# Kernel optimization log

Measured on AMD Instinct MI355X. Metric: run time of the kernel, lower is better.

Reference implementation:

```python
import jax, jax.numpy as jnp
import numpy as np

V = 32000   # vocab_size
HD = 512    # num_hiddens
B = 32      # batch
T = 128     # seq_len


def setup_inputs() -> dict:
    key = jax.random.key(0)
    ks = jax.random.split(key, 11)
    s_in = 1.0 / np.sqrt(V + HD)   # torch Linear default init bound
    s_out = 1.0 / np.sqrt(HD)

    def lin_w(k, out_f, in_f, s):
        return jax.random.uniform(k, (out_f, in_f), jnp.float32, -s, s)

    def lin_b(k, out_f, s):
        return jax.random.uniform(k, (out_f,), jnp.float32, -s, s)

    return {
        "X": jax.random.randint(ks[0], (B, T), 0, V),
        "H": jnp.zeros((B, HD), jnp.float32),
        "C": jnp.zeros((B, HD), jnp.float32),
        "Wf": lin_w(ks[1], HD, V + HD, s_in), "bf": lin_b(ks[2], HD, s_in),
        "Wi": lin_w(ks[3], HD, V + HD, s_in), "bi": lin_b(ks[4], HD, s_in),
        "Wo": lin_w(ks[5], HD, V + HD, s_in), "bo": lin_b(ks[6], HD, s_in),
        "Wc": lin_w(ks[7], HD, V + HD, s_in), "bc": lin_b(ks[8], HD, s_in),
        "Wy": lin_w(ks[9], V, HD, s_out),     "by": lin_b(ks[10], V, s_out),
    }


def reference(X, H, C, Wf, bf, Wi, bi, Wo, bo, Wc, bc, Wy, by):
    # X: [B, T] int tokens. Transposed to time-major like torch's X.T.
    Xt = X.T  # [T, B]
    hd = H.shape[1]
    v = Wf.shape[1] - hd

    def split(W):
        return W[:, :v], W[:, v:]  # input part, hidden part

    Wfx, Wfh = split(Wf)
    Wix, Wih = split(Wi)
    Wox, Woh = split(Wo)
    Wcx, Wch = split(Wc)

    # one_hot(x) @ Wx^T == row-gather of Wx^T: same math, no wasted compute.
    Ef = jnp.take(Wfx.T, Xt, axis=0) + bf  # [T, B, HD]
    Ei = jnp.take(Wix.T, Xt, axis=0) + bi
    Eo = jnp.take(Wox.T, Xt, axis=0) + bo
    Ec = jnp.take(Wcx.T, Xt, axis=0) + bc

    def step(carry, e):
        h, c = carry
        ef, ei, eo, ec = e
        f = jax.nn.sigmoid(ef + h @ Wfh.T)
        i = jax.nn.sigmoid(ei + h @ Wih.T)
        o = jax.nn.sigmoid(eo + h @ Woh.T)
        c_tilde = jnp.tanh(ec + h @ Wch.T)
        c = f * c + i * c_tilde
        h = o * jnp.tanh(c)
        return (h, c), h

    (H, C), Hs = jax.lax.scan(step, (H, C), (Ef, Ei, Eo, Ec))  # Hs: [T, B, HD]

    # per-step Y = h2out(H), then torch.cat(outputs, dim=0) -> [T*B, V]
    Y = Hs.reshape(-1, hd) @ Wy.T + by
    return Y, (H, C)
```

## Files before the change

### kernel.cpp

```cpp
#include <hip/hip_runtime.h>
#include <hip/hip_bf16.h>

#define V  32000
#define HD 512
#define BB 32
#define TT 128
#define VH 32512
#define LBLK 8
#define NBLK 256
#define GBLK (NBLK - LBLK)
#define NTILE (32 * 125)

typedef short  short8  __attribute__((ext_vector_type(8)));
typedef unsigned short u16x8 __attribute__((ext_vector_type(8)));
typedef unsigned short u16x4 __attribute__((ext_vector_type(4)));
typedef float  f32x4   __attribute__((ext_vector_type(4)));

__device__ __forceinline__ unsigned short bf16_rne(float f) {
  unsigned u = __builtin_bit_cast(unsigned, f);
  u += 0x7FFFu + ((u >> 16) & 1u);
  return (unsigned short)(u >> 16);
}

__device__ __forceinline__ void gload_lds16(const void* g, void* l) {
  __builtin_amdgcn_global_load_lds((const __attribute__((address_space(1))) void*)g,
                                   (__attribute__((address_space(3))) void*)l, 16, 0, 0);
}

__device__ __forceinline__ float sigf(float x) {
  return 1.0f / (1.0f + __expf(-x));
}
__device__ __forceinline__ float tanhf_fast(float x) {
  return 1.0f - 2.0f / (1.0f + __expf(2.0f * x));
}

__device__ __forceinline__ unsigned aload(const unsigned* p) {
  return __hip_atomic_load(p, __ATOMIC_RELAXED, __HIP_MEMORY_SCOPE_AGENT);
}
__device__ __forceinline__ void astore(unsigned* p, unsigned v) {
  __hip_atomic_store(p, v, __ATOMIC_RELAXED, __HIP_MEMORY_SCOPE_AGENT);
}
__device__ __forceinline__ unsigned aadd(unsigned* p, unsigned v) {
  return __hip_atomic_fetch_add(p, v, __ATOMIC_RELAXED, __HIP_MEMORY_SCOPE_AGENT);
}

__global__ void __launch_bounds__(512, 2) fused_all(
    const int* __restrict__ X,
    const float* __restrict__ Hin,
    const float* __restrict__ Cin,
    const float* __restrict__ Wf, const float* __restrict__ bfp,
    const float* __restrict__ Wi, const float* __restrict__ bip,
    const float* __restrict__ Wo, const float* __restrict__ bop,
    const float* __restrict__ Wc, const float* __restrict__ bcp,
    const float* __restrict__ Wy, const float* __restrict__ by,
    float* __restrict__ E,
    unsigned short* __restrict__ HsM1,
    unsigned short* __restrict__ Wyb,
    float* __restrict__ outHC,
    unsigned* __restrict__ bar,
    unsigned* __restrict__ bar2,
    unsigned* __restrict__ wbar,
    unsigned* __restrict__ eflag,
    unsigned* __restrict__ lticket,
    unsigned* __restrict__ gticket,
    float* __restrict__ Y)
{
  __shared__ __align__(16) char smem[75776];
  __shared__ int sh_role;

  const int tid = threadIdx.x;
  const int wid = tid >> 6, lane = tid & 63;
  const int fr = lane & 15, ko = lane >> 4;

  unsigned short* Hs = HsM1 + BB * HD;

  if (tid == 0) {
    unsigned xcd;
    asm volatile("s_getreg_b32 %0, hwreg(20, 0, 32)" : "=s"(xcd));
    int role = -1;
    if (xcd == 0) {
      const unsigned s = aadd(lticket, 1u);
      if (s < (unsigned)LBLK) role = (int)s;
    }
    if (role < 0) {
      const unsigned g = aadd(gticket, 1u);
      role = -(int)g - 2;
    }
    sh_role = role;
  }
  __syncthreads();
  const int role = sh_role;

  if (role >= 0) {
    short* hl = (short*)smem;
    float (*Pl)[BB][68] = (float(*)[BB][68])(smem + 32768);
    float (*cl)[64]     = (float(*)[64])(smem + 32768 + 34816);

    const int blk = role;
    const int g = wid & 3, qg = wid >> 2;

    const float* Wg = (g == 0) ? Wf : (g == 1) ? Wi : (g == 2) ? Wo : Wc;
    short8 wreg[2][16];
    #pragma unroll
    for (int n = 0; n < 2; ++n) {
      const int q = blk * 64 + qg * 32 + n * 16 + fr;
      const float* rowp = Wg + (size_t)q * VH + V;
      #pragma unroll
      for (int kk = 0; kk < 16; ++kk) {
        const float4 lo = *(const float4*)(rowp + kk * 32 + ko * 8);
        const float4 hi = *(const float4*)(rowp + kk * 32 + ko * 8 + 4);
        short8 w;
        w[0] = (short)bf16_rne(lo.x); w[1] = (short)bf16_rne(lo.y);
        w[2] = (short)bf16_rne(lo.z); w[3] = (short)bf16_rne(lo.w);
        w[4] = (short)bf16_rne(hi.x); w[5] = (short)bf16_rne(hi.y);
        w[6] = (short)bf16_rne(hi.z); w[7] = (short)bf16_rne(hi.w);
        wreg[n][kk] = w;
      }
    }

    const int e0 = tid * 4;
    const int eb = e0 >> 6, ql = e0 & 63;
    const int qglob = blk * 64 + ql;
    {
      const f32x4 c4 = *(const f32x4*)(Cin + eb * HD + qglob);
      *(f32x4*)&cl[eb][ql] = c4;
      const f32x4 h4 = *(const f32x4*)(Hin + eb * HD + qglob);
      u16x4 hq;
      #pragma unroll
      for (int j = 0; j < 4; ++j) hq[j] = bf16_rne(h4[j]);
      *(u16x4*)(HsM1 + (size_t)eb * HD + qglob) = hq;
    }
    __syncthreads();

    if (tid == 0) {
      aadd(bar, 1u);
      while (aload(bar) < (unsigned)LBLK) {}
      while (aload(&eflag[0]) < 1u) {}
    }
    __syncthreads();

    int abase[2], asw[2];
    #pragma unroll
    for (int m = 0; m < 2; ++m) {
      const int r = m * 16 + fr;
      abase[m] = r * 1024;
      asw[m] = (r & 7) << 4;
    }

    for (int t = 0; t < TT; ++t) {
      if (t > 0) {
        __syncthreads();
        if (tid == 0) {
          aadd(bar, 1u);
          const unsigned tgt = (unsigned)(LBLK * (t + 1));
          while (aload(bar) < tgt) {}
          while (aload(&eflag[t]) < 1u) {}
          if (blk == 0 && (t & 7) == 0) {
            __threadfence();
            astore(bar2, (unsigned)t);
          }
        }
        __syncthreads();
      }

      const char* hsrc = (const char*)(HsM1 + (size_t)t * (BB * HD));
      #pragma unroll
      for (int is = 0; is < 4; ++is) {
        const int i = is * 512 + tid;
        const int sb = (i >> 6) * 1024 + (((i & 63) * 16) ^ (((i >> 6) & 7) << 4));
        gload_lds16(hsrc + sb, (char*)hl + (size_t)(is * 512 + (tid & ~63)) * 16);
      }

      const float* Eb = E + ((size_t)t * 4) * BB * HD;
      const f32x4 ef = *(const f32x4*)(Eb + (size_t)(0 * BB + eb) * HD + qglob);
      const f32x4 ei = *(const f32x4*)(Eb + (size_t)(1 * BB + eb) * HD + qglob);
      const f32x4 eo = *(const f32x4*)(Eb + (size_t)(2 * BB + eb) * HD + qglob);
      const f32x4 ec = *(const f32x4*)(Eb + (size_t)(3 * BB + eb) * HD + qglob);

      __syncthreads();

      f32x4 acc[2][2];
      #pragma unroll
      for (int m = 0; m < 2; ++m)
        #pragma unroll
        for (int n = 0; n < 2; ++n)
          acc[m][n] = (f32x4){0.f, 0.f, 0.f, 0.f};

      #pragma unroll
      for (int kk = 0; kk < 16; ++kk) {
        const int off = kk * 64 + ko * 16;
        const short8 a0 = *(const short8*)((const char*)hl + abase[0] + (off ^ asw[0]));
        const short8 a1 = *(const short8*)((const char*)hl + abase[1] + (off ^ asw[1]));
        acc[0][0] = __builtin_amdgcn_mfma_f32_16x16x32_bf16(a0, wreg[0][kk], acc[0][0], 0, 0, 0);
        acc[1][0] = __builtin_amdgcn_mfma_f32_16x16x32_bf16(a1, wreg[0][kk], acc[1][0], 0, 0, 0);
        acc[0][1] = __builtin_amdgcn_mfma_f32_16x16x32_bf16(a0, wreg[1][kk], acc[0][1], 0, 0, 0);
        acc[1][1] = __builtin_amdgcn_mfma_f32_16x16x32_bf16(a1, wreg[1][kk], acc[1][1], 0, 0, 0);
      }

      #pragma unroll
      for (int m = 0; m < 2; ++m)
        #pragma unroll
        for (int n = 0; n < 2; ++n)
          #pragma unroll
          for (int j = 0; j < 4; ++j)
            Pl[g][m * 16 + ko * 4 + j][qg * 32 + n * 16 + fr] = acc[m][n][j];
      __syncthreads();

      const f32x4 pf4 = *(const f32x4*)&Pl[0][eb][ql];
      const f32x4 pi4 = *(const f32x4*)&Pl[1][eb][ql];
      const f32x4 po4 = *(const f32x4*)&Pl[2][eb][ql];
      const f32x4 pc4 = *(const f32x4*)&Pl[3][eb][ql];
      const f32x4 cold = *(const f32x4*)&cl[eb][ql];
      f32x4 cnew, hnew;
      u16x4 hq;
      #pragma unroll
      for (int j = 0; j < 4; ++j) {
        const float fg = sigf(pf4[j] + ef[j]);
        const float ig = sigf(pi4[j] + ei[j]);
        const float og = sigf(po4[j] + eo[j]);
        const float ct = tanhf_fast(pc4[j] + ec[j]);
        const float cn = fg * cold[j] + ig * ct;
        const float hv = og * tanhf_fast(cn);
        cnew[j] = cn;
        hnew[j] = hv;
        hq[j] = bf16_rne(hv);
      }
      *(f32x4*)&cl[eb][ql] = cnew;
      *(u16x4*)(Hs + ((size_t)t * BB + eb) * HD + qglob) = hq;
      if (t == TT - 1) {
        *(f32x4*)(outHC + (size_t)eb * HD + qglob) = hnew;
        *(f32x4*)(outHC + (size_t)BB * HD + (size_t)eb * HD + qglob) = cnew;
      }
    }

    __syncthreads();
    if (tid == 0) {
      aadd(bar, 1u);
      if (blk == 0) {
        while (aload(bar) < (unsigned)(LBLK * (TT + 1))) {}
        __threadfence();
        astore(bar2, (unsigned)TT);
      }
    }
  } else {
    unsigned short* As = (unsigned short*)smem;
    unsigned short* Bs = (unsigned short*)(smem + 16384);
    int* xs            = (int*)(smem + 49152);

    const int gid = -role - 2;

    if (gid < TT) {
      const int tch = gid;
      if (tid < BB) xs[tid] = X[tid * TT + tch];
      __syncthreads();
      const int q = tid;
      float* Erow = E + ((size_t)tch * 4) * BB * HD;
      #pragma unroll
      for (int g = 0; g < 4; ++g) {
        const float* W = (g == 0) ? Wf : (g == 1) ? Wi : (g == 2) ? Wo : Wc;
        const float* bsrc = (g == 0) ? bfp : (g == 1) ? bip : (g == 2) ? bop : bcp;
        const float bias = bsrc[q];
        const float* wq = W + (size_t)q * VH;
        #pragma unroll 4
        for (int b = 0; b < BB; ++b) {
          const float v = __builtin_nontemporal_load(wq + xs[b]);
          Erow[(size_t)(g * BB + b) * HD + q] = v + bias;
        }
      }
      __syncthreads();
      if (tid == 0) {
        __threadfence();
        astore(&eflag[tch], 1u);
      }
    }

    {
      const size_t n = (size_t)V * HD;
      for (size_t i = ((size_t)gid * 512 + tid) * 8; i < n;
           i += (size_t)GBLK * 512 * 8) {
        const f32x4 a = __builtin_nontemporal_load((const f32x4*)(Wy + i));
        const f32x4 b = __builtin_nontemporal_load((const f32x4*)(Wy + i + 4));
        u16x8 o;
        o[0] = bf16_rne(a[0]); o[1] = bf16_rne(a[1]); o[2] = bf16_rne(a[2]); o[3] = bf16_rne(a[3]);
        o[4] = bf16_rne(b[0]); o[5] = bf16_rne(b[1]); o[6] = bf16_rne(b[2]); o[7] = bf16_rne(b[3]);
        *(u16x8*)(Wyb + i) = o;
      }
      __syncthreads();
      if (tid == 0) {
        __threadfence();
        aadd(wbar, 1u);
        while (aload(wbar) < (unsigned)GBLK)
          __builtin_amdgcn_s_sleep(2);
      }
      __syncthreads();
    }

    const int wr = wid >> 2, wc = wid & 3;

    for (int tile = gid; tile < NTILE; tile += GBLK) {
      const int bm = tile / 125, bn = tile % 125;
      const int row0 = bm << 7, col0 = bn << 8;

      if (tid == 0) {
        const unsigned need = (unsigned)(4 * bm + 4);
        while (aload(bar2) < need)
          __builtin_amdgcn_s_sleep(2);
      }
      __syncthreads();

      f32x4 acc[4][4];
      #pragma unroll
      for (int m = 0; m < 4; ++m)
        #pragma unroll
        for (int n = 0; n < 4; ++n)
          acc[m][n] = (f32x4){0.f, 0.f, 0.f, 0.f};

      for (int kt = 0; kt < 8; ++kt) {
        const int k0 = kt << 6;
        #pragma unroll
        for (int is = 0; is < 2; ++is) {
          const int id = is * 512 + tid;
          const int r = id >> 3;
          const int c = (id & 7) ^ (r & 7);
          gload_lds16(Hs + (size_t)(row0 + r) * 512 + k0 + c * 8,
                      &As[(is * 512 + (tid & ~63)) * 8]);
        }
        #pragma unroll
        for (int is = 0; is < 4; ++is) {
          const int id = is * 512 + tid;
          const int r = id >> 3;
          const int c = (id & 7) ^ (r & 7);
          gload_lds16(Wyb + (size_t)(col0 + r) * 512 + k0 + c * 8,
                      &Bs[(is * 512 + (tid & ~63)) * 8]);
        }
        __syncthreads();
        #pragma unroll
        for (int kk = 0; kk < 2; ++kk) {
          short8 af[4], bfr[4];
          #pragma unroll
          for (int m = 0; m < 4; ++m) {
            const int r = (wr << 6) + (m << 4) + fr;
            const int c = ((kk << 2) | ko) ^ (r & 7);
            af[m] = *(const short8*)&As[r * 64 + c * 8];
          }
          #pragma unroll
          for (int n = 0; n < 4; ++n) {
            const int r = (wc << 6) + (n << 4) + fr;
            const int c = ((kk << 2) | ko) ^ (r & 7);
            bfr[n] = *(const short8*)&Bs[r * 64 + c * 8];
          }
          #pragma unroll
          for (int m = 0; m < 4; ++m)
            #pragma unroll
            for (int n = 0; n < 4; ++n)
              acc[m][n] = __builtin_amdgcn_mfma_f32_16x16x32_bf16(
                  af[m], bfr[n], acc[m][n], 0, 0, 0);
        }
        __syncthreads();
      }

      const int rgrp = lane >> 4;
      #pragma unroll
      for (int n = 0; n < 4; ++n) {
        const int col = col0 + (wc << 6) + (n << 4) + fr;
        const float bias = by[col];
        #pragma unroll
        for (int m = 0; m < 4; ++m) {
          const int rowb = row0 + (wr << 6) + (m << 4) + (rgrp << 2);
          #pragma unroll
          for (int j = 0; j < 4; ++j) {
            __builtin_nontemporal_store(acc[m][n][j] + bias,
                                        &Y[(size_t)(rowb + j) * V + col]);
          }
        }
      }
    }
  }
}

extern "C" void kernel_launch(void* const* d_in, const int* in_sizes, int n_in,
                              void* d_out, int out_size, void* d_ws, size_t ws_size,
                              hipStream_t stream)
{
  const int*   X  = (const int*)  d_in[0];
  const float* H  = (const float*)d_in[1];
  const float* C  = (const float*)d_in[2];
  const float* Wf = (const float*)d_in[3];
  const float* bf = (const float*)d_in[4];
  const float* Wi = (const float*)d_in[5];
  const float* bi = (const float*)d_in[6];
  const float* Wo = (const float*)d_in[7];
  const float* bo = (const float*)d_in[8];
  const float* Wc = (const float*)d_in[9];
  const float* bc = (const float*)d_in[10];
  const float* Wy = (const float*)d_in[11];
  const float* by = (const float*)d_in[12];

  float* Y = (float*)d_out;
  float* outHC = Y + (size_t)TT * BB * V;

  char* ws = (char*)d_ws;
  float* E              = (float*)ws;
  unsigned short* Wyb   = (unsigned short*)(ws + 33554432);
  unsigned short* HsM1  = (unsigned short*)(ws + 66322432);
  unsigned* bar         = (unsigned*)(ws + 70549504);
  unsigned* bar2        = (unsigned*)(ws + 70549504 + 64);
  unsigned* wbar        = (unsigned*)(ws + 70549504 + 128);
  unsigned* lticket     = (unsigned*)(ws + 70549504 + 192);
  unsigned* gticket     = (unsigned*)(ws + 70549504 + 256);
  unsigned* eflag       = (unsigned*)(ws + 70549504 + 320);

  (void)hipMemsetAsync(bar, 0, 1024, stream);

  {
    const int* X_p = X;
    const float *H_p = H, *C_p = C;
    const float *Wf_p = Wf, *bf_p = bf, *Wi_p = Wi, *bi_p = bi;
    const float *Wo_p = Wo, *bo_p = bo, *Wc_p = Wc, *bc_p = bc;
    const float *Wy_p = Wy, *by_p = by;
    float* E_p = E;
    unsigned short* HsM1_p = HsM1;
    unsigned short* Wyb_p = Wyb;
    float* outHC_p = outHC;
    unsigned *bar_p = bar, *bar2_p = bar2, *wbar_p = wbar, *eflag_p = eflag;
    unsigned *lticket_p = lticket, *gticket_p = gticket;
    float* Y_p = Y;
    void* args[] = {(void*)&X_p, (void*)&H_p, (void*)&C_p,
                    (void*)&Wf_p, (void*)&bf_p, (void*)&Wi_p, (void*)&bi_p,
                    (void*)&Wo_p, (void*)&bo_p, (void*)&Wc_p, (void*)&bc_p,
                    (void*)&Wy_p, (void*)&by_p,
                    (void*)&E_p, (void*)&HsM1_p, (void*)&Wyb_p, (void*)&outHC_p,
                    (void*)&bar_p, (void*)&bar2_p, (void*)&wbar_p, (void*)&eflag_p,
                    (void*)&lticket_p, (void*)&gticket_p,
                    (void*)&Y_p};
    (void)hipLaunchCooperativeKernel((void*)fused_all, dim3(NBLK), dim3(512), args, 0, stream);
  }
}
```

Measured before the change: 900.3 us.

## Replace LSTM step barrier with per-block flags and register-resident gate layout

```diff
diff --git a/kernel.cpp b/kernel.cpp
--- a/kernel.cpp
+++ b/kernel.cpp
@@ -57,9 +57,9 @@
     unsigned short* __restrict__ HsM1,
     unsigned short* __restrict__ Wyb,
     float* __restrict__ outHC,
-    unsigned* __restrict__ bar,
     unsigned* __restrict__ bar2,
     unsigned* __restrict__ wbar,
+    unsigned* __restrict__ bflag,
     unsigned* __restrict__ eflag,
     unsigned* __restrict__ lticket,
     unsigned* __restrict__ gticket,
@@ -71,6 +71,7 @@
   const int tid = threadIdx.x;
   const int wid = tid >> 6, lane = tid & 63;
   const int fr = lane & 15, ko = lane >> 4;
+  const int rowgrp = lane >> 4;
 
   unsigned short* Hs = HsM1 + BB * HD;
 
@@ -92,19 +93,16 @@
   const int role = sh_role;
 
   if (role >= 0) {
-    short* hl = (short*)smem;
-    float (*Pl)[BB][68] = (float(*)[BB][68])(smem + 32768);
-    float (*cl)[64]     = (float(*)[64])(smem + 32768 + 34816);
-
     const int blk = role;
-    const int g = wid & 3, qg = wid >> 2;
-
-    const float* Wg = (g == 0) ? Wf : (g == 1) ? Wi : (g == 2) ? Wo : Wc;
+    const int qb = blk * 64 + wid * 8;
+
     short8 wreg[2][16];
     #pragma unroll
-    for (int n = 0; n < 2; ++n) {
-      const int q = blk * 64 + qg * 32 + n * 16 + fr;
-      const float* rowp = Wg + (size_t)q * VH + V;
+    for (int mt = 0; mt < 2; ++mt) {
+      const int qA = qb + mt * 4 + (fr >> 2);
+      const int gA = fr & 3;
+      const float* WgA = (gA == 0) ? Wf : (gA == 1) ? Wi : (gA == 2) ? Wo : Wc;
+      const float* rowp = WgA + (size_t)qA * VH + V;
       #pragma unroll
       for (int kk = 0; kk < 16; ++kk) {
         const float4 lo = *(const float4*)(rowp + kk * 32 + ko * 8);
@@ -114,130 +112,106 @@
         w[2] = (short)bf16_rne(lo.z); w[3] = (short)bf16_rne(lo.w);
         w[4] = (short)bf16_rne(hi.x); w[5] = (short)bf16_rne(hi.y);
         w[6] = (short)bf16_rne(hi.z); w[7] = (short)bf16_rne(hi.w);
-        wreg[n][kk] = w;
-      }
-    }
-
-    const int e0 = tid * 4;
-    const int eb = e0 >> 6, ql = e0 & 63;
-    const int qglob = blk * 64 + ql;
-    {
-      const f32x4 c4 = *(const f32x4*)(Cin + eb * HD + qglob);
-      *(f32x4*)&cl[eb][ql] = c4;
-      const f32x4 h4 = *(const f32x4*)(Hin + eb * HD + qglob);
-      u16x4 hq;
-      #pragma unroll
-      for (int j = 0; j < 4; ++j) hq[j] = bf16_rne(h4[j]);
-      *(u16x4*)(HsM1 + (size_t)eb * HD + qglob) = hq;
-    }
+        wreg[mt][kk] = w;
+      }
+    }
+
+    float creg[2][2];
+    #pragma unroll
+    for (int mt = 0; mt < 2; ++mt)
+      #pragma unroll
+      for (int nt = 0; nt < 2; ++nt) {
+        const int b = nt * 16 + fr;
+        const int q = qb + mt * 4 + rowgrp;
+        creg[mt][nt] = Cin[b * HD + q];
+        HsM1[(size_t)b * HD + q] = bf16_rne(Hin[b * HD + q]);
+      }
     __syncthreads();
-
-    if (tid == 0) {
-      aadd(bar, 1u);
-      while (aload(bar) < (unsigned)LBLK) {}
-      while (aload(&eflag[0]) < 1u) {}
-    }
-    __syncthreads();
-
-    int abase[2], asw[2];
-    #pragma unroll
-    for (int m = 0; m < 2; ++m) {
-      const int r = m * 16 + fr;
-      abase[m] = r * 1024;
-      asw[m] = (r & 7) << 4;
-    }
+    if (wid == 0 && lane == 0) astore(&bflag[blk * 16], 1u);
 
     for (int t = 0; t < TT; ++t) {
-      if (t > 0) {
-        __syncthreads();
-        if (tid == 0) {
-          aadd(bar, 1u);
-          const unsigned tgt = (unsigned)(LBLK * (t + 1));
-          while (aload(bar) < tgt) {}
-          while (aload(&eflag[t]) < 1u) {}
-          if (blk == 0 && (t & 7) == 0) {
-            __threadfence();
-            astore(bar2, (unsigned)t);
+      {
+        const unsigned* pa = (lane < 8) ? (bflag + lane * 16)
+                           : (lane == 8) ? (eflag + t) : bflag;
+        const unsigned tgt = (lane < 8) ? (unsigned)(t + 1)
+                           : (lane == 8) ? 4u : 0u;
+        while (true) {
+          const unsigned v = aload(pa);
+          if (__all((int)(v >= tgt))) break;
+        }
+      }
+      if (blk == 0 && wid == 0 && lane == 0 && t && !(t & 7)) {
+        __threadfence();
+        astore(bar2, (unsigned)t);
+      }
+
+      f32x4 eld[2][2];
+      {
+        const float* Ebase = E + (size_t)t * BB * HD * 4;
+        #pragma unroll
+        for (int mt = 0; mt < 2; ++mt)
+          #pragma unroll
+          for (int nt = 0; nt < 2; ++nt) {
+            const int b = nt * 16 + fr;
+            const int q = qb + mt * 4 + rowgrp;
+            eld[mt][nt] = *(const f32x4*)(Ebase + ((size_t)b * HD + q) * 4);
           }
-        }
-        __syncthreads();
-      }
-
-      const char* hsrc = (const char*)(HsM1 + (size_t)t * (BB * HD));
-      #pragma unroll
-      for (int is = 0; is < 4; ++is) {
-        const int i = is * 512 + tid;
-        const int sb = (i >> 6) * 1024 + (((i & 63) * 16) ^ (((i >> 6) & 7) << 4));
-        gload_lds16(hsrc + sb, (char*)hl + (size_t)(is * 512 + (tid & ~63)) * 16);
-      }
-
-      const float* Eb = E + ((size_t)t * 4) * BB * HD;
-      const f32x4 ef = *(const f32x4*)(Eb + (size_t)(0 * BB + eb) * HD + qglob);
-      const f32x4 ei = *(const f32x4*)(Eb + (size_t)(1 * BB + eb) * HD + qglob);
-      const f32x4 eo = *(const f32x4*)(Eb + (size_t)(2 * BB + eb) * HD + qglob);
-      const f32x4 ec = *(const f32x4*)(Eb + (size_t)(3 * BB + eb) * HD + qglob);
-
-      __syncthreads();
-
+      }
+
+      const char* hb0 = (const char*)HsM1 + (size_t)t * (BB * HD * 2)
+                      + fr * (HD * 2) + ko * 16;
+      const char* hb1 = hb0 + 16 * (HD * 2);
       f32x4 acc[2][2];
       #pragma unroll
-      for (int m = 0; m < 2; ++m)
-        #pragma unroll
-        for (int n = 0; n < 2; ++n)
-          acc[m][n] = (f32x4){0.f, 0.f, 0.f, 0.f};
-
+      for (int mt = 0; mt < 2; ++mt)
+        #pragma unroll
+        for (int nt = 0; nt < 2; ++nt)
+          acc[mt][nt] = (f32x4){0.f, 0.f, 0.f, 0.f};
       #pragma unroll
       for (int kk = 0; kk < 16; ++kk) {
-        const int off = kk * 64 + ko * 16;
-        const short8 a0 = *(const short8*)((const char*)hl + abase[0] + (off ^ asw[0]));
-        const short8 a1 = *(const short8*)((const char*)hl + abase[1] + (off ^ asw[1]));
-        acc[0][0] = __builtin_amdgcn_mfma_f32_16x16x32_bf16(a0, wreg[0][kk], acc[0][0], 0, 0, 0);
-        acc[1][0] = __builtin_amdgcn_mfma_f32_16x16x32_bf16(a1, wreg[0][kk], acc[1][0], 0, 0, 0);
-        acc[0][1] = __builtin_amdgcn_mfma_f32_16x16x32_bf16(a0, wreg[1][kk], acc[0][1], 0, 0, 0);
-        acc[1][1] = __builtin_amdgcn_mfma_f32_16x16x32_bf16(a1, wreg[1][kk], acc[1][1], 0, 0, 0);
-      }
-
-      #pragma unroll
-      for (int m = 0; m < 2; ++m)
-        #pragma unroll
-        for (int n = 0; n < 2; ++n)
-          #pragma unroll
-          for (int j = 0; j < 4; ++j)
-            Pl[g][m * 16 + ko * 4 + j][qg * 32 + n * 16 + fr] = acc[m][n][j];
-      __syncthreads();
-
-      const f32x4 pf4 = *(const f32x4*)&Pl[0][eb][ql];
-      const f32x4 pi4 = *(const f32x4*)&Pl[1][eb][ql];
-      const f32x4 po4 = *(const f32x4*)&Pl[2][eb][ql];
-      const f32x4 pc4 = *(const f32x4*)&Pl[3][eb][ql];
-      const f32x4 cold = *(const f32x4*)&cl[eb][ql];
-      f32x4 cnew, hnew;
-      u16x4 hq;
-      #pragma unroll
-      for (int j = 0; j < 4; ++j) {
-        const float fg = sigf(pf4[j] + ef[j]);
-        const float ig = sigf(pi4[j] + ei[j]);
-        const float og = sigf(po4[j] + eo[j]);
-        const float ct = tanhf_fast(pc4[j] + ec[j]);
-        const float cn = fg * cold[j] + ig * ct;
-        const float hv = og * tanhf_fast(cn);
-        cnew[j] = cn;
-        hnew[j] = hv;
-        hq[j] = bf16_rne(hv);
-      }
-      *(f32x4*)&cl[eb][ql] = cnew;
-      *(u16x4*)(Hs + ((size_t)t * BB + eb) * HD + qglob) = hq;
-      if (t == TT - 1) {
-        *(f32x4*)(outHC + (size_t)eb * HD + qglob) = hnew;
-        *(f32x4*)(outHC + (size_t)BB * HD + (size_t)eb * HD + qglob) = cnew;
-      }
-    }
-
-    __syncthreads();
-    if (tid == 0) {
-      aadd(bar, 1u);
-      if (blk == 0) {
-        while (aload(bar) < (unsigned)(LBLK * (TT + 1))) {}
+        const short8 b0 = *(const short8*)(hb0 + kk * 64);
+        const short8 b1 = *(const short8*)(hb1 + kk * 64);
+        acc[0][0] = __builtin_amdgcn_mfma_f32_16x16x32_bf16(wreg[0][kk], b0, acc[0][0], 0, 0, 0);
+        acc[0][1] = __builtin_amdgcn_mfma_f32_16x16x32_bf16(wreg[0][kk], b1, acc[0][1], 0, 0, 0);
+        acc[1][0] = __builtin_amdgcn_mfma_f32_16x16x32_bf16(wreg[1][kk], b0, acc[1][0], 0, 0, 0);
+        acc[1][1] = __builtin_amdgcn_mfma_f32_16x16x32_bf16(wreg[1][kk], b1, acc[1][1], 0, 0, 0);
+      }
+
+      unsigned short* hstore = HsM1 + (size_t)(t + 1) * (BB * HD);
+      #pragma unroll
+      for (int mt = 0; mt < 2; ++mt)
+        #pragma unroll
+        for (int nt = 0; nt < 2; ++nt) {
+          const int b = nt * 16 + fr;
+          const int q = qb + mt * 4 + rowgrp;
+          const f32x4 a = acc[mt][nt];
+          const f32x4 e4 = eld[mt][nt];
+          const float fg = sigf(a[0] + e4[0]);
+          const float ig = sigf(a[1] + e4[1]);
+          const float og = sigf(a[2] + e4[2]);
+          const float ct = tanhf_fast(a[3] + e4[3]);
+          const float cn = fg * creg[mt][nt] + ig * ct;
+          const float hv = og * tanhf_fast(cn);
+          creg[mt][nt] = cn;
+          hstore[(size_t)b * HD + q] = bf16_rne(hv);
+          if (t == TT - 1) {
+            outHC[(size_t)b * HD + q] = hv;
+            outHC[(size_t)BB * HD + b * HD + q] = cn;
+          }
+        }
+
+      __syncthreads();
+      if (wid == 0 && lane == 0) astore(&bflag[blk * 16], (unsigned)(t + 2));
+    }
+
+    if (wid == 0) {
+      const unsigned* pa = (lane < 8) ? (bflag + lane * 16) : bflag;
+      const unsigned tgt = (lane < 8) ? (unsigned)(TT + 1) : 0u;
+      while (true) {
+        const unsigned v = aload(pa);
+        if (__all((int)(v >= tgt))) break;
+      }
+      if (blk == 0 && lane == 0) {
         __threadfence();
         astore(bar2, (unsigned)TT);
       }
@@ -249,28 +223,28 @@
 
     const int gid = -role - 2;
 
-    if (gid < TT) {
-      const int tch = gid;
-      if (tid < BB) xs[tid] = X[tid * TT + tch];
+    for (int u = gid; u < 4 * TT; u += GBLK) {
+      const int tg = u >> 2, qtr = u & 3;
+      if (tid < 8) xs[tid] = X[(qtr * 8 + tid) * TT + tg];
       __syncthreads();
       const int q = tid;
-      float* Erow = E + ((size_t)tch * 4) * BB * HD;
-      #pragma unroll
-      for (int g = 0; g < 4; ++g) {
-        const float* W = (g == 0) ? Wf : (g == 1) ? Wi : (g == 2) ? Wo : Wc;
-        const float* bsrc = (g == 0) ? bfp : (g == 1) ? bip : (g == 2) ? bop : bcp;
-        const float bias = bsrc[q];
-        const float* wq = W + (size_t)q * VH;
-        #pragma unroll 4
-        for (int b = 0; b < BB; ++b) {
-          const float v = __builtin_nontemporal_load(wq + xs[b]);
-          Erow[(size_t)(g * BB + b) * HD + q] = v + bias;
-        }
+      const float b0v = bfp[q], b1v = bip[q], b2v = bop[q], b3v = bcp[q];
+      float* Ebase = E + (size_t)tg * BB * HD * 4;
+      #pragma unroll
+      for (int b = 0; b < 8; ++b) {
+        const int xv = xs[b];
+        f32x4 ev;
+        ev[0] = __builtin_nontemporal_load(Wf + (size_t)q * VH + xv) + b0v;
+        ev[1] = __builtin_nontemporal_load(Wi + (size_t)q * VH + xv) + b1v;
+        ev[2] = __builtin_nontemporal_load(Wo + (size_t)q * VH + xv) + b2v;
+        ev[3] = __builtin_nontemporal_load(Wc + (size_t)q * VH + xv) + b3v;
+        __builtin_nontemporal_store(ev,
+            (f32x4*)(Ebase + ((size_t)(qtr * 8 + b) * HD + q) * 4));
       }
       __syncthreads();
       if (tid == 0) {
         __threadfence();
-        astore(&eflag[tch], 1u);
+        aadd(&eflag[tg], 1u);
       }
     }
 
@@ -403,14 +377,15 @@
   float* E              = (float*)ws;
   unsigned short* Wyb   = (unsigned short*)(ws + 33554432);
   unsigned short* HsM1  = (unsigned short*)(ws + 66322432);
-  unsigned* bar         = (unsigned*)(ws + 70549504);
-  unsigned* bar2        = (unsigned*)(ws + 70549504 + 64);
-  unsigned* wbar        = (unsigned*)(ws + 70549504 + 128);
-  unsigned* lticket     = (unsigned*)(ws + 70549504 + 192);
-  unsigned* gticket     = (unsigned*)(ws + 70549504 + 256);
-  unsigned* eflag       = (unsigned*)(ws + 70549504 + 320);
-
-  (void)hipMemsetAsync(bar, 0, 1024, stream);
+  char* ctrl            = ws + 70549504;
+  unsigned* lticket     = (unsigned*)(ctrl + 0);
+  unsigned* gticket     = (unsigned*)(ctrl + 64);
+  unsigned* bar2        = (unsigned*)(ctrl + 128);
+  unsigned* wbar        = (unsigned*)(ctrl + 192);
+  unsigned* bflag       = (unsigned*)(ctrl + 256);
+  unsigned* eflag       = (unsigned*)(ctrl + 768);
+
+  (void)hipMemsetAsync(ctrl, 0, 2048, stream);
 
   {
     const int* X_p = X;
@@ -422,7 +397,7 @@
     unsigned short* HsM1_p = HsM1;
     unsigned short* Wyb_p = Wyb;
     float* outHC_p = outHC;
-    unsigned *bar_p = bar, *bar2_p = bar2, *wbar_p = wbar, *eflag_p = eflag;
+    unsigned *bar2_p = bar2, *wbar_p = wbar, *bflag_p = bflag, *eflag_p = eflag;
     unsigned *lticket_p = lticket, *gticket_p = gticket;
     float* Y_p = Y;
     void* args[] = {(void*)&X_p, (void*)&H_p, (void*)&C_p,
@@ -430,7 +405,7 @@
                     (void*)&Wo_p, (void*)&bo_p, (void*)&Wc_p, (void*)&bc_p,
                     (void*)&Wy_p, (void*)&by_p,
                     (void*)&E_p, (void*)&HsM1_p, (void*)&Wyb_p, (void*)&outHC_p,
-                    (void*)&bar_p, (void*)&bar2_p, (void*)&wbar_p, (void*)&eflag_p,
+                    (void*)&bar2_p, (void*)&wbar_p, (void*)&bflag_p, (void*)&eflag_p,
                     (void*)&lticket_p, (void*)&gticket_p,
                     (void*)&Y_p};
     (void)hipLaunchCooperativeKernel((void*)fused_all, dim3(NBLK), dim3(512), args, 0, stream);
```

New measurement: 1.531 ms. 1.7x slower.
